# Kernel optimization log

Measured on AMD Instinct MI355X. Metric: run time of the kernel, lower is better.

## Reference

```python
import jax, jax.numpy as jnp
import numpy as np

N, E, C_IN, C_OUT = 50000, 800000, 64, 64
BN_EPS = 1e-5


def _batchnorm(h, gamma, beta):
    # Training-mode BatchNorm1d: batch statistics over dim 0, biased variance.
    mean = h.mean(axis=0)
    var = h.var(axis=0)  # ddof=0, matches PyTorch normalization stats
    return gamma * (h - mean) * jax.lax.rsqrt(var + BN_EPS) + beta


def setup_inputs() -> dict:
    key = jax.random.key(0)
    ks = jax.random.split(key, 6)
    x = jax.random.normal(ks[0], (N, C_IN), dtype=jnp.float32)
    edge_index = jax.random.randint(ks[1], (2, E), 0, N, dtype=jnp.int32)
    edge_weight = jax.random.uniform(ks[2], (E,), dtype=jnp.float32)
    s1 = 1.0 / np.sqrt(C_IN).astype(np.float32)
    s2 = 1.0 / np.sqrt(2 * C_IN).astype(np.float32)
    pool_W = jax.random.uniform(ks[3], (C_IN, C_IN), jnp.float32, -s1, s1)
    pool_b = jnp.zeros((C_IN,), jnp.float32)
    final_W = jax.random.uniform(ks[4], (2 * C_IN, C_OUT), jnp.float32, -s2, s2)
    final_b = jnp.zeros((C_OUT,), jnp.float32)
    return {
        "x": x,
        "edge_index": edge_index,
        "edge_weight": edge_weight,
        "pool_W": pool_W,
        "pool_b": pool_b,
        "bn_pool_gamma": jnp.ones((C_IN,), jnp.float32),
        "bn_pool_beta": jnp.zeros((C_IN,), jnp.float32),
        "final_W": final_W,
        "final_b": final_b,
        "bn_final_gamma": jnp.ones((C_OUT,), jnp.float32),
        "bn_final_beta": jnp.zeros((C_OUT,), jnp.float32),
        "coef": jnp.float32(0.5),
    }


def reference(x, edge_index, edge_weight, pool_W, pool_b, bn_pool_gamma,
              bn_pool_beta, final_W, final_b, bn_final_gamma, bn_final_beta,
              coef):
    src, dst = edge_index[0], edge_index[1]
    # gather src node features, scale by edge weight  -> [E, C_IN]
    edge_feat = x[src] * (1.0 + coef * edge_weight[:, None])
    pooled = edge_feat @ pool_W + pool_b              # [E, C_IN]
    pooled = jax.nn.relu(_batchnorm(pooled, bn_pool_gamma, bn_pool_beta))
    # scatter-max into destination nodes; empty segments -> 0 (pooled >= 0)
    agg = jax.ops.segment_max(pooled, dst, num_segments=x.shape[0])
    agg = jnp.maximum(agg, 0.0)                       # fill -inf (empty) with 0
    h = jnp.concatenate([x, agg], axis=-1) @ final_W + final_b  # [N, C_OUT]
    h = _batchnorm(h, bn_final_gamma, bn_final_beta)
    return jax.nn.relu(h)
```

## Files before the change

kernel.cpp:

```cpp
#include <hip/hip_runtime.h>
#include <hip/hip_fp16.h>
#include <math.h>
#include <float.h>

#define BN_EPS 1e-5f
#define SLOTS 64


typedef __attribute__((ext_vector_type(8))) short bf16x8;
typedef __attribute__((ext_vector_type(4))) float f32x4;

__device__ inline unsigned short f2bf(float f) {
    unsigned u = __float_as_uint(f);
    return (unsigned short)((u + 0x7fffu + ((u >> 16) & 1u)) >> 16);
}
__device__ inline float bf2f(unsigned short h) {
    return __uint_as_float(((unsigned)h) << 16);
}

__global__ __launch_bounds__(256) void k_scatter(const int* __restrict__ src,
                          const int* __restrict__ dst,
                          const float* __restrict__ w, const float* __restrict__ coef_p,
                          int* __restrict__ cnt, unsigned* __restrict__ csr, int E) {
    int i = blockIdx.x * blockDim.x + threadIdx.x;
    if (i >= E) return;
    const float coef = *coef_p;
    int sn = src[i], tn = dst[i];
    float s = fmaf(coef, w[i], 1.0f);
    unsigned hs = (unsigned)__half_as_ushort(__float2half(s));
    int pos = atomicAdd(&cnt[tn], 1);
    if (pos < SLOTS) csr[(size_t)tn * SLOTS + pos] = ((unsigned)sn << 16) | hs;
}

__global__ __launch_bounds__(256, 4) void k_gemm_pool(const float* __restrict__ x,
                            const float* __restrict__ W,
                            unsigned short* __restrict__ ybf, int nrows) {
    __shared__ unsigned short Wt[64 * 72];
    for (int i = threadIdx.x; i < 64 * 64; i += 256) {
        int k = i >> 6, n = i & 63;
        Wt[n * 72 + k] = f2bf(W[i]);
    }
    __syncthreads();
    const int lane = threadIdx.x & 63;
    const int wave = threadIdx.x >> 6;
    const int quad = lane >> 4;
    const int ln = lane & 15;
    bf16x8 Bf[2][4];
#pragma unroll
    for (int kc = 0; kc < 2; ++kc)
#pragma unroll
        for (int ct = 0; ct < 4; ++ct)
            Bf[kc][ct] = *(const bf16x8*)&Wt[(ct * 16 + ln) * 72 + kc * 32 + quad * 8];
    const int T = (nrows + 15) >> 4;
    const int gw = blockIdx.x * 4 + wave;
    const int nw = gridDim.x * 4;
    for (int t = gw; t < T; t += nw) {
        const int row = t * 16 + ln;
        bf16x8 af[2];
        if (row < nrows) {
            const float* xr = x + (size_t)row * 64;
#pragma unroll
            for (int kc = 0; kc < 2; ++kc) {
                float4 p = *(const float4*)(xr + kc * 32 + quad * 8);
                float4 q = *(const float4*)(xr + kc * 32 + quad * 8 + 4);
                bf16x8 a;
                a[0] = (short)f2bf(p.x); a[1] = (short)f2bf(p.y);
                a[2] = (short)f2bf(p.z); a[3] = (short)f2bf(p.w);
                a[4] = (short)f2bf(q.x); a[5] = (short)f2bf(q.y);
                a[6] = (short)f2bf(q.z); a[7] = (short)f2bf(q.w);
                af[kc] = a;
            }
        } else {
            bf16x8 z;
#pragma unroll
            for (int j = 0; j < 8; ++j) z[j] = 0;
            af[0] = z; af[1] = z;
        }
        f32x4 acc[4];
#pragma unroll
        for (int ct = 0; ct < 4; ++ct) { acc[ct][0]=0.f; acc[ct][1]=0.f; acc[ct][2]=0.f; acc[ct][3]=0.f; }
#pragma unroll
        for (int ct = 0; ct < 4; ++ct) {
            acc[ct] = __builtin_amdgcn_mfma_f32_16x16x32_bf16(af[0], Bf[0][ct], acc[ct], 0, 0, 0);
            acc[ct] = __builtin_amdgcn_mfma_f32_16x16x32_bf16(af[1], Bf[1][ct], acc[ct], 0, 0, 0);
        }
#pragma unroll
        for (int r = 0; r < 4; ++r) {
            int ro = t * 16 + quad * 4 + r;
            if (ro < nrows) {
#pragma unroll
                for (int ct = 0; ct < 4; ++ct)
                    ybf[(size_t)ro * 64 + ct * 16 + ln] = f2bf(acc[ct][r]);
            }
        }
    }
}

__global__ __launch_bounds__(256) void k_gather_max(const unsigned short* __restrict__ ybf,
                             const unsigned* __restrict__ csr, const int* __restrict__ cnt,
                             float* __restrict__ M, float* __restrict__ partials, int nrows) {
    int t = blockIdx.x * blockDim.x + threadIdx.x;
    int node = t >> 4;
    int sub = threadIdx.x & 15;
    int rg = threadIdx.x >> 4;
    int c0 = sub * 4;
    size_t base = (size_t)node * SLOTS;
    int dg = 0;
    if (node < nrows) { dg = cnt[node]; if (dg > SLOTS) dg = SLOTS; }
    float m0 = -FLT_MAX, m1 = -FLT_MAX, m2 = -FLT_MAX, m3 = -FLT_MAX;
    float s1[4] = {0, 0, 0, 0}, s2[4] = {0, 0, 0, 0};
    for (int k0 = 0; k0 < dg; k0 += 16) {
        int kk = k0 + sub;
        unsigned pk = (kk < dg) ? csr[base + kk] : 0u;
        int cnt16 = dg - k0; if (cnt16 > 16) cnt16 = 16;
        if (cnt16 == 16) {
            ushort4 uv[16];
            float sv[16];
#pragma unroll
            for (int j = 0; j < 16; ++j) {
                unsigned r = (unsigned)__shfl((int)pk, j, 16);
                sv[j] = __half2float(__ushort_as_half((unsigned short)(r & 0xffffu)));
                uv[j] = *(const ushort4*)&ybf[(size_t)(r >> 16) * 64 + c0];
            }
#pragma unroll
            for (int j = 0; j < 16; ++j) {
                float v0 = sv[j] * bf2f(uv[j].x), v1 = sv[j] * bf2f(uv[j].y);
                float v2 = sv[j] * bf2f(uv[j].z), v3 = sv[j] * bf2f(uv[j].w);
                m0 = fmaxf(m0, v0); s1[0] += v0; s2[0] = fmaf(v0, v0, s2[0]);
                m1 = fmaxf(m1, v1); s1[1] += v1; s2[1] = fmaf(v1, v1, s2[1]);
                m2 = fmaxf(m2, v2); s1[2] += v2; s2[2] = fmaf(v2, v2, s2[2]);
                m3 = fmaxf(m3, v3); s1[3] += v3; s2[3] = fmaf(v3, v3, s2[3]);
            }
        } else {
            for (int j = 0; j < cnt16; ++j) {
                unsigned r = (unsigned)__shfl((int)pk, j, 16);
                int sn = r >> 16;
                float sv = __half2float(__ushort_as_half((unsigned short)(r & 0xffffu)));
                ushort4 uv = *(const ushort4*)&ybf[(size_t)sn * 64 + c0];
                float v0 = sv * bf2f(uv.x), v1 = sv * bf2f(uv.y);
                float v2 = sv * bf2f(uv.z), v3 = sv * bf2f(uv.w);
                m0 = fmaxf(m0, v0); s1[0] += v0; s2[0] = fmaf(v0, v0, s2[0]);
                m1 = fmaxf(m1, v1); s1[1] += v1; s2[1] = fmaf(v1, v1, s2[1]);
                m2 = fmaxf(m2, v2); s1[2] += v2; s2[2] = fmaf(v2, v2, s2[2]);
                m3 = fmaxf(m3, v3); s1[3] += v3; s2[3] = fmaf(v3, v3, s2[3]);
            }
        }
    }
    if (node < nrows)
        *(float4*)&M[(size_t)node * 64 + c0] = make_float4(m0, m1, m2, m3);
    __shared__ float red[16][68];
#pragma unroll
    for (int j = 0; j < 4; ++j) red[rg][c0 + j] = s1[j];
    __syncthreads();
    if (rg == 0) {
#pragma unroll
        for (int j = 0; j < 4; ++j) {
            float tt = 0.0f;
            for (int r = 0; r < 16; ++r) tt += red[r][c0 + j];
            partials[(size_t)blockIdx.x * 128 + c0 + j] = tt;
        }
    }
    __syncthreads();
#pragma unroll
    for (int j = 0; j < 4; ++j) red[rg][c0 + j] = s2[j];
    __syncthreads();
    if (rg == 0) {
#pragma unroll
        for (int j = 0; j < 4; ++j) {
            float tt = 0.0f;
            for (int r = 0; r < 16; ++r) tt += red[r][c0 + j];
            partials[(size_t)blockIdx.x * 128 + 64 + c0 + j] = tt;
        }
    }
}

__global__ __launch_bounds__(256) void k_red1(const float* __restrict__ partials, int P,
                                              float* __restrict__ p2) {
    int c = threadIdx.x & 127;
    int half = threadIdx.x >> 7;
    float acc = 0.0f;
    for (int r = blockIdx.x * 2 + half; r < P; r += 256)
        acc += partials[(size_t)r * 128 + c];
    __shared__ float sh[256];
    sh[threadIdx.x] = acc;
    __syncthreads();
    if (half == 0) p2[(size_t)blockIdx.x * 128 + c] = sh[c] + sh[128 + c];
}

__global__ __launch_bounds__(1024) void k_red2(const float* __restrict__ p2,
                             const float* __restrict__ pool_b, const float* __restrict__ gamma,
                             const float* __restrict__ beta, float invE,
                             float* __restrict__ coef) {
    int c = threadIdx.x & 127;
    int seg = threadIdx.x >> 7;
    float acc = 0.0f;
    for (int r = seg; r < 128; r += 8) acc += p2[(size_t)r * 128 + c];
    __shared__ float red[8][128];
    red[seg][c] = acc;
    __syncthreads();
    if (seg == 0) {
        float tt = 0.0f;
#pragma unroll
        for (int s = 0; s < 8; ++s) tt += red[s][c];
        red[0][c] = tt;
    }
    __syncthreads();
    if (threadIdx.x < 64) {
        int c0 = threadIdx.x;
        float S1 = red[0][c0], S2 = red[0][64 + c0];
        float s1 = S1 * invE;
        float b = pool_b[c0];
        float mean = s1 + b;
        float ex2 = S2 * invE + 2.0f * b * s1 + b * b;
        float var = ex2 - mean * mean;
        float a = gamma[c0] * rsqrtf(var + BN_EPS);
        coef[c0] = a;
        coef[64 + c0] = beta[c0] - a * s1;
    }
}

__global__ __launch_bounds__(1024) void k_red2f(const float* __restrict__ p2,
                             const float* __restrict__ gamma, const float* __restrict__ beta,
                             float invN, float* __restrict__ coef) {
    int c = threadIdx.x & 127;
    int seg = threadIdx.x >> 7;
    float acc = 0.0f;
    for (int r = seg; r < 128; r += 8) acc += p2[(size_t)r * 128 + c];
    __shared__ float red[8][128];
    red[seg][c] = acc;
    __syncthreads();
    if (seg == 0) {
        float tt = 0.0f;
#pragma unroll
        for (int s = 0; s < 8; ++s) tt += red[s][c];
        red[0][c] = tt;
    }
    __syncthreads();
    if (threadIdx.x < 64) {
        int c0 = threadIdx.x;
        float mean = red[0][c0] * invN;
        float var = red[0][64 + c0] * invN - mean * mean;
        float a = gamma[c0] * rsqrtf(var + BN_EPS);
        coef[c0] = a;
        coef[64 + c0] = beta[c0] - a * mean;
    }
}

__global__ __launch_bounds__(256, 2) void k_final_gemm(const float* __restrict__ x,
                             const float* __restrict__ M, const float* __restrict__ coef,
                             const float* __restrict__ W, const float* __restrict__ b,
                             float* __restrict__ h, float* __restrict__ partials, int nrows) {
    __shared__ unsigned short Wt[64 * 136];
    __shared__ float hp[128];
    for (int i = threadIdx.x; i < 128 * 64; i += 256) {
        int k = i >> 6, n = i & 63;
        Wt[n * 136 + k] = f2bf(W[i]);
    }
    if (threadIdx.x < 128) hp[threadIdx.x] = 0.0f;
    __syncthreads();
    const int lane = threadIdx.x & 63;
    const int wave = threadIdx.x >> 6;
    const int quad = lane >> 4;
    const int ln = lane & 15;
    bf16x8 Bf[4][4];
#pragma unroll
    for (int kc = 0; kc < 4; ++kc)
#pragma unroll
        for (int ct = 0; ct < 4; ++ct)
            Bf[kc][ct] = *(const bf16x8*)&Wt[(ct * 16 + ln) * 136 + kc * 32 + quad * 8];
    float bias[4];
#pragma unroll
    for (int ct = 0; ct < 4; ++ct) bias[ct] = b[ct * 16 + ln];
    float ca[2][8], cd[2][8];
#pragma unroll
    for (int g = 0; g < 2; ++g) {
        int ch = g * 32 + quad * 8;
#pragma unroll
        for (int j = 0; j < 8; ++j) {
            ca[g][j] = coef[ch + j];
            cd[g][j] = coef[64 + ch + j];
        }
    }
    float ls1[4] = {0, 0, 0, 0}, ls2[4] = {0, 0, 0, 0};
    const int T = (nrows + 15) >> 4;
    const int gw = blockIdx.x * 4 + wave;
    const int nw = gridDim.x * 4;
    for (int t = gw; t < T; t += nw) {
        const int row = t * 16 + ln;
        bf16x8 af[4];
        if (row < nrows) {
            const float* xr = x + (size_t)row * 64;
#pragma unroll
            for (int kc = 0; kc < 2; ++kc) {
                float4 p = *(const float4*)(xr + kc * 32 + quad * 8);
                float4 q = *(const float4*)(xr + kc * 32 + quad * 8 + 4);
                bf16x8 a;
                a[0] = (short)f2bf(p.x); a[1] = (short)f2bf(p.y);
                a[2] = (short)f2bf(p.z); a[3] = (short)f2bf(p.w);
                a[4] = (short)f2bf(q.x); a[5] = (short)f2bf(q.y);
                a[6] = (short)f2bf(q.z); a[7] = (short)f2bf(q.w);
                af[kc] = a;
            }
            const float* mr = M + (size_t)row * 64;
#pragma unroll
            for (int g = 0; g < 2; ++g) {
                const float* mp = mr + g * 32 + quad * 8;
                float4 p = *(const float4*)mp;
                float4 q = *(const float4*)(mp + 4);
                float v[8] = {p.x, p.y, p.z, p.w, q.x, q.y, q.z, q.w};
                bf16x8 a;
#pragma unroll
                for (int j = 0; j < 8; ++j)
                    a[j] = (short)f2bf(fmaxf(fmaf(ca[g][j], v[j], cd[g][j]), 0.0f));
                af[2 + g] = a;
            }
        } else {
            bf16x8 z;
#pragma unroll
            for (int j = 0; j < 8; ++j) z[j] = 0;
#pragma unroll
            for (int kc = 0; kc < 4; ++kc) af[kc] = z;
        }
        f32x4 acc[4];
#pragma unroll
        for (int ct = 0; ct < 4; ++ct) { acc[ct][0]=0.f; acc[ct][1]=0.f; acc[ct][2]=0.f; acc[ct][3]=0.f; }
#pragma unroll
        for (int kc = 0; kc < 4; ++kc)
#pragma unroll
            for (int ct = 0; ct < 4; ++ct)
                acc[ct] = __builtin_amdgcn_mfma_f32_16x16x32_bf16(af[kc], Bf[kc][ct], acc[ct], 0, 0, 0);
#pragma unroll
        for (int r = 0; r < 4; ++r) {
            int ro = t * 16 + quad * 4 + r;
            if (ro < nrows) {
#pragma unroll
                for (int ct = 0; ct < 4; ++ct) {
                    float hv = acc[ct][r] + bias[ct];
                    h[(size_t)ro * 64 + ct * 16 + ln] = hv;
                    ls1[ct] += hv;
                    ls2[ct] = fmaf(hv, hv, ls2[ct]);
                }
            }
        }
    }
#pragma unroll
    for (int ct = 0; ct < 4; ++ct) {
        atomicAdd(&hp[ct * 16 + ln], ls1[ct]);
        atomicAdd(&hp[64 + ct * 16 + ln], ls2[ct]);
    }
    __syncthreads();
    if (threadIdx.x < 128)
        partials[(size_t)blockIdx.x * 128 + threadIdx.x] = hp[threadIdx.x];
}

__global__ __launch_bounds__(256) void k_bn_out(const float* __restrict__ h,
                         const float* __restrict__ coef,
                         float* __restrict__ out, int nrows) {
    const int idx = blockIdx.x * blockDim.x + threadIdx.x;
    const int total = nrows * 16;
    if (idx >= total) return;
    const int c0 = (idx & 15) * 4;
    const float4 hv = *(const float4*)(h + (size_t)idx * 4);
    float4 o;
    float* op = (float*)&o;
    const float* hp = (const float*)&hv;
#pragma unroll
    for (int j = 0; j < 4; ++j) {
        const int c = c0 + j;
        op[j] = fmaxf(fmaf(coef[c], hp[j], coef[64 + c]), 0.0f);
    }
    *(float4*)(out + (size_t)idx * 4) = o;
}

extern "C" void kernel_launch(void* const* d_in, const int* in_sizes, int n_in,
                              void* d_out, int out_size, void* d_ws, size_t ws_size,
                              hipStream_t stream) {
    const float* x       = (const float*)d_in[0];
    const int*   eidx    = (const int*)d_in[1];
    const float* ew      = (const float*)d_in[2];
    const float* pool_W  = (const float*)d_in[3];
    const float* pool_b  = (const float*)d_in[4];
    const float* g1      = (const float*)d_in[5];
    const float* b1      = (const float*)d_in[6];
    const float* final_W = (const float*)d_in[7];
    const float* final_b = (const float*)d_in[8];
    const float* g2      = (const float*)d_in[9];
    const float* b2      = (const float*)d_in[10];
    const float* coef    = (const float*)d_in[11];

    const int N = in_sizes[0] / 64;
    const int E = in_sizes[1] / 2;
    const int* src = eidx;
    const int* dst = eidx + E;

    const int PG  = (N * 16 + 255) / 256;
    const int T   = (N + 15) / 16;
    const int nbT = (T + 3) / 4;

    unsigned* ws = (unsigned*)d_ws;
    int*   cnt      = (int*)ws;
    float* bncoef   = (float*)(ws + (size_t)N);
    float* coef2    = (float*)(ws + (size_t)N + 128);
    float* p2       = (float*)(ws + (size_t)N + 256);
    float* p2F      = p2 + 16384;
    float* partialsG= p2F + 16384;
    float* partialsF= partialsG + (size_t)PG * 128;
    unsigned short* ybf = (unsigned short*)(partialsF + (size_t)nbT * 128);
    unsigned* csrF  = (unsigned*)ybf + (size_t)32 * N;
    float* M        = (float*)(csrF + (size_t)SLOTS * N);

    hipMemsetAsync(cnt, 0, (size_t)N * 4, stream);

    const int nb256 = (E + 255) / 256;

    k_scatter<<<nb256, 256, 0, stream>>>(src, dst, ew, coef, cnt, csrF, E);
    k_gemm_pool<<<nbT, 256, 0, stream>>>(x, pool_W, ybf, N);
    k_gather_max<<<PG, 256, 0, stream>>>(ybf, csrF, cnt, M, partialsG, N);
    k_red1   <<<128, 256, 0, stream>>>(partialsG, PG, p2);
    k_red2   <<<1, 1024, 0, stream>>>(p2, pool_b, g1, b1, 1.0f / (float)E, bncoef);
    k_final_gemm<<<nbT, 256, 0, stream>>>(x, M, bncoef, final_W, final_b,
                                          (float*)d_out, partialsF, N);
    k_red1   <<<128, 256, 0, stream>>>(partialsF, nbT, p2F);
    k_red2f  <<<1, 1024, 0, stream>>>(p2F, g2, b2, 1.0f / (float)N, coef2);
    k_bn_out <<<(N * 16 + 255) / 256, 256, 0, stream>>>((const float*)d_out, coef2,
                                                        (float*)d_out, N);
}
```

Baseline: 217.0 us.

## Fuse edge scatter and pooling GEMM into one launch with block specialization

Merges the CSR-building scatter kernel and the node-level pooling GEMM into a single kernel. The first 256 blocks run a grid-stride scatter that handles four edges per thread with vectorized int4/float4 loads, and the remaining blocks run the GEMM. This removes one kernel launch and lets the atomic-heavy scatter overlap with the compute-bound GEMM. The cost is that the scatter blocks now carry the GEMM's shared-memory allocation and launch bounds, and the fixed block count of 256 may leave the scatter undersubscribed.

Result: no change. 216.9 us (-0.0%).

```diff
diff --git a/kernel.cpp b/kernel.cpp
--- a/kernel.cpp
+++ b/kernel.cpp
@@ -5,6 +5,7 @@
 
 #define BN_EPS 1e-5f
 #define SLOTS 64
+#define SB 256
 
 
 typedef __attribute__((ext_vector_type(8))) short bf16x8;
@@ -18,24 +19,52 @@
     return __uint_as_float(((unsigned)h) << 16);
 }
 
-__global__ __launch_bounds__(256) void k_scatter(const int* __restrict__ src,
-                          const int* __restrict__ dst,
-                          const float* __restrict__ w, const float* __restrict__ coef_p,
-                          int* __restrict__ cnt, unsigned* __restrict__ csr, int E) {
-    int i = blockIdx.x * blockDim.x + threadIdx.x;
-    if (i >= E) return;
-    const float coef = *coef_p;
-    int sn = src[i], tn = dst[i];
-    float s = fmaf(coef, w[i], 1.0f);
-    unsigned hs = (unsigned)__half_as_ushort(__float2half(s));
-    int pos = atomicAdd(&cnt[tn], 1);
-    if (pos < SLOTS) csr[(size_t)tn * SLOTS + pos] = ((unsigned)sn << 16) | hs;
-}
-
-__global__ __launch_bounds__(256, 4) void k_gemm_pool(const float* __restrict__ x,
-                            const float* __restrict__ W,
-                            unsigned short* __restrict__ ybf, int nrows) {
+__global__ __launch_bounds__(256, 4) void k_scatter_gemm(
+        const int* __restrict__ src, const int* __restrict__ dst,
+        const float* __restrict__ w, const float* __restrict__ coef_p,
+        int* __restrict__ cnt, unsigned* __restrict__ csr, int E,
+        const float* __restrict__ x, const float* __restrict__ W,
+        unsigned short* __restrict__ ybf, int nrows, int gemmGrid) {
     __shared__ unsigned short Wt[64 * 72];
+    if (blockIdx.x < SB) {
+        const float coef = *coef_p;
+        const int tid = blockIdx.x * 256 + threadIdx.x;
+        const int stride4 = SB * 256 * 4;
+        for (int base = tid * 4; base < E; base += stride4) {
+            if (base + 3 < E) {
+                int4   s4 = *(const int4*)(src + base);
+                int4   d4 = *(const int4*)(dst + base);
+                float4 w4 = *(const float4*)(w + base);
+                int sn[4] = {s4.x, s4.y, s4.z, s4.w};
+                int dn[4] = {d4.x, d4.y, d4.z, d4.w};
+                float wv[4] = {w4.x, w4.y, w4.z, w4.w};
+                unsigned hs[4];
+                int pos[4];
+#pragma unroll
+                for (int j = 0; j < 4; ++j) {
+                    float s = fmaf(coef, wv[j], 1.0f);
+                    hs[j] = (unsigned)__half_as_ushort(__float2half(s));
+                    pos[j] = atomicAdd(&cnt[dn[j]], 1);
+                }
+#pragma unroll
+                for (int j = 0; j < 4; ++j)
+                    if (pos[j] < SLOTS)
+                        csr[(size_t)dn[j] * SLOTS + pos[j]] =
+                            ((unsigned)sn[j] << 16) | hs[j];
+            } else {
+                for (int i = base; i < E; ++i) {
+                    int sn = src[i], tn = dst[i];
+                    float s = fmaf(coef, w[i], 1.0f);
+                    unsigned hs = (unsigned)__half_as_ushort(__float2half(s));
+                    int pos = atomicAdd(&cnt[tn], 1);
+                    if (pos < SLOTS)
+                        csr[(size_t)tn * SLOTS + pos] = ((unsigned)sn << 16) | hs;
+                }
+            }
+        }
+        return;
+    }
+    const int bid = blockIdx.x - SB;
     for (int i = threadIdx.x; i < 64 * 64; i += 256) {
         int k = i >> 6, n = i & 63;
         Wt[n * 72 + k] = f2bf(W[i]);
@@ -52,8 +81,8 @@
         for (int ct = 0; ct < 4; ++ct)
             Bf[kc][ct] = *(const bf16x8*)&Wt[(ct * 16 + ln) * 72 + kc * 32 + quad * 8];
     const int T = (nrows + 15) >> 4;
-    const int gw = blockIdx.x * 4 + wave;
-    const int nw = gridDim.x * 4;
+    const int gw = bid * 4 + wave;
+    const int nw = gemmGrid * 4;
     for (int t = gw; t < T; t += nw) {
         const int row = t * 16 + ln;
         bf16x8 af[2];
@@ -411,10 +440,8 @@
 
     hipMemsetAsync(cnt, 0, (size_t)N * 4, stream);
 
-    const int nb256 = (E + 255) / 256;
-
-    k_scatter<<<nb256, 256, 0, stream>>>(src, dst, ew, coef, cnt, csrF, E);
-    k_gemm_pool<<<nbT, 256, 0, stream>>>(x, pool_W, ybf, N);
+    k_scatter_gemm<<<SB + nbT, 256, 0, stream>>>(src, dst, ew, coef, cnt, csrF, E,
+                                                 x, pool_W, ybf, N, nbT);
     k_gather_max<<<PG, 256, 0, stream>>>(ybf, csrF, cnt, M, partialsG, N);
     k_red1   <<<128, 256, 0, stream>>>(partialsG, PG, p2);
     k_red2   <<<1, 1024, 0, stream>>>(p2, pool_b, g1, b1, 1.0f / (float)E, bncoef);
```
